# Performance work log

Measured on AMD Instinct MI355X. Metric: run time of the kernel, lower is better.

Reference implementation:

```python
import jax, jax.numpy as jnp
import numpy as np

H, W = 256, 336
FLOW_SCALING = float(max(H, W))  # max(config['loader']['resolution'])
REG_WEIGHT = 0.001               # config['loss']['flow_regul_weight']
B, N = 8, 262144


def setup_inputs() -> dict:
    key = jax.random.key(0)
    k1, k2, k3, k4, k5 = jax.random.split(key, 5)
    # small flow so a reasonable fraction of warped events stays in-bounds
    flow = 0.05 * jax.random.normal(k1, (B, 2, H, W), dtype=jnp.float32)
    ys = jax.random.randint(k2, (B, N), 0, H).astype(jnp.float32)
    xs = jax.random.randint(k3, (B, N), 0, W).astype(jnp.float32)
    ts = jax.random.uniform(k4, (B, N), dtype=jnp.float32)  # normalized timestamps in [0,1]
    pol = jax.random.randint(k5, (B, N), 0, 2)
    # event layout per the code: (ts, y, x, p)
    event_list = jnp.stack([ts, ys, xs, pol.astype(jnp.float32) * 2.0 - 1.0], axis=-1)
    pol_mask = jnp.stack([(pol == 1), (pol == 0)], axis=-1).astype(jnp.float32)  # [B,N,2]
    return {"flow": flow, "event_list": event_list, "pol_mask": pol_mask}


def _get_interpolation(events, event_flow, tref):
    # warped event coords (y, x): [B, N, 2]
    warped = events[:, :, 1:3] + (tref - events[:, :, 0:1]) * event_flow * FLOW_SCALING
    top_y = jnp.floor(warped[:, :, 0:1])
    bot_y = jnp.floor(warped[:, :, 0:1] + 1.0)
    left_x = jnp.floor(warped[:, :, 1:2])
    right_x = jnp.floor(warped[:, :, 1:2] + 1.0)
    # four bilinear corners stacked along event dim -> [B, 4N, 2]
    idx = jnp.concatenate([
        jnp.concatenate([top_y, left_x], -1),
        jnp.concatenate([top_y, right_x], -1),
        jnp.concatenate([bot_y, left_x], -1),
        jnp.concatenate([bot_y, right_x], -1)], axis=1)
    warped4 = jnp.tile(warped, (1, 4, 1))
    weights = jnp.maximum(0.0, 1.0 - jnp.abs(warped4 - idx))
    mask = ((idx[:, :, 0:1] >= 0) & (idx[:, :, 0:1] < H)
            & (idx[:, :, 1:2] >= 0) & (idx[:, :, 1:2] < W)).astype(weights.dtype)
    idx = idx * mask          # unfeasible indices -> 0
    weights = weights * mask  # unfeasible weights -> 0
    flat_idx = (idx[:, :, 0] * W + idx[:, :, 1]).astype(jnp.int32)  # [B, 4N]
    w = jnp.prod(weights, axis=-1, keepdims=True)                    # [B, 4N, 1]
    return flat_idx, w


def _interpolate(flat_idx, weights, polarity_mask):
    # scatter-add bilinear weights into an H*W image, per batch element
    w = (weights * polarity_mask)[:, :, 0]  # [B, 4N]
    return jax.vmap(lambda i, v: jax.ops.segment_sum(v, i, num_segments=H * W))(flat_idx, w)


def reference(flow, event_list, pol_mask):
    pol4 = jnp.tile(pol_mask, (1, 4, 1))              # [B, 4N, 2]
    ts4 = jnp.tile(event_list[:, :, 0:1], (1, 4, 1))  # [B, 4N, 1]
    # gather flow at original event pixel locations
    flow_idx = (event_list[:, :, 1] * W + event_list[:, :, 2]).astype(jnp.int32)  # [B, N]
    flow_flat = flow.reshape(flow.shape[0], 2, -1)
    event_flowy = jnp.take_along_axis(flow_flat[:, 1, :], flow_idx, axis=1)
    event_flowx = jnp.take_along_axis(flow_flat[:, 0, :], flow_idx, axis=1)
    event_flow = jnp.stack([event_flowy, event_flowx], axis=-1)  # [B, N, 2] (y, x)

    loss = jnp.float32(0.0)
    # forward warp (tref=1, avg ts) and backward warp (tref=0, avg 1-ts)
    for tref, tgrad in ((1.0, ts4), (0.0, 1.0 - ts4)):
        idx, wts = _get_interpolation(event_list, event_flow, tref)
        for p in range(2):  # positive / negative polarity
            pm = pol4[:, :, p:p + 1]
            iwe = _interpolate(idx, wts, pm)
            iwe_ts = _interpolate(idx, wts * tgrad, pm)
            loss = loss + jnp.sum((iwe_ts / (iwe + 1e-9)) ** 2)

    # charbonnier flow smoothness
    flow_dx = flow[:, :, :-1, :] - flow[:, :, 1:, :]
    flow_dy = flow[:, :, :, :-1] - flow[:, :, :, 1:]
    smooth = jnp.sum(jnp.sqrt(flow_dx ** 2 + 1e-6)) + jnp.sum(jnp.sqrt(flow_dy ** 2 + 1e-6))
    return loss + REG_WEIGHT * smooth
```

## Files before the change

kernel.cpp:

```cpp
#include <hip/hip_runtime.h>

#define HH 256
#define WW 336
#define HWPIX (HH * WW)
#define BATCH 8
#define NEV 262144
#define NEV_SHIFT 18
#define FLOW_SCALING 336.0f
#define REG_WEIGHT 0.001f

#define BANDS 32
#define BANDSHIFT 3
#define BANDROWS 8
#define NBINS (2 * BATCH * BANDS)
#define CAP 14336
#define GSTRIDE 16

#define BE_THREADS 512
#define EVPT 2
#define EV_PER_BLOCK (BE_THREADS * EVPT)
#define MAXITEMS 4096

#define HTILE (BANDROWS * WW)
#define NBLK_ACC NBINS

#define GCOUNT_BYTES (NBINS * GSTRIDE * 4)
#define ITEMS_BYTES ((size_t)NBINS * CAP * 8)

__device__ __forceinline__ float wave_reduce_sum(float v) {
    #pragma unroll
    for (int o = 32; o > 0; o >>= 1) v += __shfl_down(v, o, 64);
    return v;
}

__device__ __forceinline__ float charb(float d) { return sqrtf(d * d + 1e-6f); }

__global__ __launch_bounds__(256)
void flow_prep(const float* __restrict__ flow,
               unsigned int* __restrict__ gcount, float* __restrict__ loss_acc,
               unsigned int* __restrict__ done_count,
               float* __restrict__ smooth_partial) {
    __shared__ float red[4];
    int tid = threadIdx.x;
    if (blockIdx.x == 0) {
        for (int i = tid; i < NBINS * GSTRIDE; i += 256) gcount[i] = 0u;
        if (tid == 0) { *loss_acc = 0.0f; *done_count = 0u; }
    }

    const int N4 = BATCH * HWPIX / 4;
    const int H4 = HWPIX / 4;
    const int W4 = WW / 4;
    float v = 0.0f;
    for (int i = blockIdx.x * 256 + tid; i < N4; i += gridDim.x * 256) {
        int b = i / H4, u = i - b * H4;
        int row = u / W4, c4 = u - row * W4;
        const float4* ch0 = (const float4*)(flow + (size_t)b * 2 * HWPIX);
        const float4* ch1 = ch0 + H4;
        float4 a0 = ch0[u];
        float4 a1 = ch1[u];

        if (row < HH - 1) {
            float4 d0 = ch0[u + W4];
            float4 d1 = ch1[u + W4];
            v += charb(a0.x - d0.x) + charb(a0.y - d0.y) +
                 charb(a0.z - d0.z) + charb(a0.w - d0.w) +
                 charb(a1.x - d1.x) + charb(a1.y - d1.y) +
                 charb(a1.z - d1.z) + charb(a1.w - d1.w);
        }
        v += charb(a0.x - a0.y) + charb(a0.y - a0.z) + charb(a0.z - a0.w) +
             charb(a1.x - a1.y) + charb(a1.y - a1.z) + charb(a1.z - a1.w);
        if (c4 < W4 - 1) {
            float r0 = ((const float*)ch0)[4 * u + 4];
            float r1 = ((const float*)ch1)[4 * u + 4];
            v += charb(a0.w - r0) + charb(a1.w - r1);
        }
    }
    v = wave_reduce_sum(v);
    if ((tid & 63) == 0) red[tid >> 6] = v;
    __syncthreads();
    if (tid < 4) {
        float r = red[tid];
        r += __shfl_down(r, 2, 64);
        r += __shfl_down(r, 1, 64);
        if (tid == 0) smooth_partial[blockIdx.x] = r;
    }
}

__global__ __launch_bounds__(BE_THREADS)
void bin_events(const float* __restrict__ flow,
                const float4* __restrict__ ev,
                unsigned int* __restrict__ gcount,
                uint2* __restrict__ items) {
    __shared__ int lcnt[64];
    __shared__ int loff[64];
    __shared__ int gbase[64];
    __shared__ int stotal;
    __shared__ __align__(16) unsigned long long sval[MAXITEMS];

    int tid = threadIdx.x;
    if (tid < 64) lcnt[tid] = 0;
    __syncthreads();

    int base = blockIdx.x * EV_PER_BLOCK;
    int b = base >> NEV_SHIFT;
    const float* fxp = flow + (size_t)b * 2 * HWPIX;
    const float* fyp = fxp + HWPIX;

    unsigned int pkv[EVPT][2];
    unsigned int hiA[EVPT][2], hiB[EVPT][2];
    int rkA[EVPT][2], rkB[EVPT][2];

    #pragma unroll
    for (int e = 0; e < EVPT; ++e) {
        int bn = base + e * BE_THREADS + tid;
        float4 ee = ev[bn];
        float t = ee.x, y = ee.y, x = ee.z;
        unsigned int p = (ee.w > 0.0f) ? 0u : 1u;

        int iy = (int)y, ix = (int)x;
        int off = iy * WW + ix;
        float fx = fxp[off];
        float fy = fyp[off];

        #pragma unroll
        for (int tr = 0; tr < 2; ++tr) {
            rkA[e][tr] = -1; rkB[e][tr] = -1;
            float tref  = tr ? 0.0f : 1.0f;
            float tg    = tr ? (1.0f - t) : t;
            float dtS = (tref - t) * FLOW_SCALING;
            float wy = fmaf(dtS, fy, y);
            float wx = fmaf(dtS, fx, x);
            if (!(wx > -1.0f && wx < (float)WW)) continue;
            if (!(wy > -1.0f && wy < (float)HH)) continue;

            int ty = (int)floorf(wy);
            int band0 = -1, band1 = -1;
            if (ty >= 0 && ty < HH) band0 = ty >> BANDSHIFT;
            int r1 = ty + 1;
            if (r1 >= 0 && r1 < HH) {
                int bb = r1 >> BANDSHIFT;
                if (bb != band0) band1 = bb;
            }

            unsigned int qx = (unsigned int)(fmaf(wx, 2048.0f, 2048.5f));
            unsigned int qt = (unsigned int)(tg * 2047.0f + 0.5f);
            pkv[e][tr] = (qx << 12) | (qt << 1) | p;

            if (band0 >= 0) {
                float wyrel = wy - (float)(band0 * BANDROWS - 1);
                unsigned int qy = (unsigned int)fmaf(wyrel, 2048.0f, 0.5f);
                int lb = tr * BANDS + band0;
                hiA[e][tr] = qy | ((unsigned int)lb << 16);
                rkA[e][tr] = atomicAdd(&lcnt[lb], 1);
            }
            if (band1 >= 0) {
                float wyrel = wy - (float)(band1 * BANDROWS - 1);
                unsigned int qy = (unsigned int)fmaf(wyrel, 2048.0f, 0.5f);
                int lb = tr * BANDS + band1;
                hiB[e][tr] = qy | ((unsigned int)lb << 16);
                rkB[e][tr] = atomicAdd(&lcnt[lb], 1);
            }
        }
    }
    __syncthreads();

    if (tid < 64) {
        int c = lcnt[tid];
        int xg = c;
        #pragma unroll
        for (int o = 1; o < 64; o <<= 1) {
            int yv = __shfl_up(xg, o, 64);
            if (tid >= o) xg += yv;
        }
        loff[tid] = xg - c;
        if (tid == 63) stotal = xg;
        int gbin = ((tid >> 5) * BATCH + b) * BANDS + (tid & 31);
        gbase[tid] = c > 0 ? (int)atomicAdd(&gcount[gbin * GSTRIDE],
                                            (unsigned int)c) : 0;
    }
    __syncthreads();

    #pragma unroll
    for (int e = 0; e < EVPT; ++e) {
        #pragma unroll
        for (int tr = 0; tr < 2; ++tr) {
            if (rkA[e][tr] >= 0) {
                int lb = (hiA[e][tr] >> 16) & 63;
                sval[loff[lb] + rkA[e][tr]] =
                    (unsigned long long)pkv[e][tr] |
                    ((unsigned long long)hiA[e][tr] << 32);
            }
            if (rkB[e][tr] >= 0) {
                int lb = (hiB[e][tr] >> 16) & 63;
                sval[loff[lb] + rkB[e][tr]] =
                    (unsigned long long)pkv[e][tr] |
                    ((unsigned long long)hiB[e][tr] << 32);
            }
        }
    }
    __syncthreads();

    int total = stotal;
    for (int i = tid * 2; i < total; i += 2 * BE_THREADS) {
        uint4 two = *(const uint4*)&sval[i];
        unsigned int pk0 = two.x, h0 = two.y;
        unsigned int qy0 = h0 & 0xffffu;
        int lb0 = (h0 >> 16) & 63;
        int gs0 = gbase[lb0] + (i - loff[lb0]);
        int gbin0 = ((lb0 >> 5) * BATCH + b) * BANDS + (lb0 & 31);

        if ((i + 1) < total) {
            unsigned int pk1 = two.z, h1 = two.w;
            unsigned int qy1 = h1 & 0xffffu;
            int lb1 = (h1 >> 16) & 63;
            int gs1 = gbase[lb1] + (i + 1 - loff[lb1]);
            if (lb1 == lb0 && (gs0 & 1) == 0 && gs1 < CAP) {
                *(uint4*)(items + (size_t)gbin0 * CAP + gs0) =
                    make_uint4(pk0, qy0, pk1, qy1);
                continue;
            }
            int gbin1 = ((lb1 >> 5) * BATCH + b) * BANDS + (lb1 & 31);
            if (gs1 < CAP) items[(size_t)gbin1 * CAP + gs1] = make_uint2(pk1, qy1);
        }
        if (gs0 < CAP) items[(size_t)gbin0 * CAP + gs0] = make_uint2(pk0, qy0);
    }
}

__device__ __forceinline__ unsigned int pack_w(float w, float tg) {
    unsigned int lo16 = (unsigned int)fmaf(w, 1024.0f, 0.5f);
    unsigned int hi16 = (unsigned int)fmaf(w * tg, 1024.0f, 0.5f);
    return lo16 | (hi16 << 16);
}

__device__ __forceinline__ void accum_item(unsigned int* __restrict__ sA,
                                           unsigned int* __restrict__ sB,
                                           unsigned int pk, unsigned int qy) {
    float wx = (float)(pk >> 12) * (1.0f / 2048.0f) - 1.0f;
    float tg = (float)((pk >> 1) & 2047u) * (1.0f / 2047.0f);
    int p = pk & 1u;

    int rowq = qy >> 11;
    float fy = (float)(qy & 2047u) * (1.0f / 2048.0f);
    int row_top = rowq - 1;

    float lxf = floorf(wx);
    float fxx = wx - lxf;
    int lx = (int)lxf;

    unsigned int* A  = sA + p * HTILE;
    unsigned int* Bb = sB + p * HTILE;

    #pragma unroll
    for (int a = 0; a < 2; ++a) {
        int ry = row_top + a;
        if ((unsigned)ry >= (unsigned)BANDROWS) continue;
        float wrow = a ? fy : (1.0f - fy);
        int rb = ry * WW;
        if (lx >= 0 && lx + 1 < WW) {
            unsigned int pl = pack_w(wrow * (1.0f - fxx), tg);
            unsigned int pr = pack_w(wrow * fxx, tg);
            unsigned long long v =
                (unsigned long long)pl | ((unsigned long long)pr << 32);
            if ((lx & 1) == 0) {
                atomicAdd((unsigned long long*)(A + rb + lx), v);
            } else {
                atomicAdd((unsigned long long*)(Bb + rb + lx - 1), v);
            }
        } else if (lx == -1) {
            atomicAdd(&A[rb], pack_w(wrow * fxx, tg));
        } else if (lx == WW - 1) {
            atomicAdd(&A[rb + lx], pack_w(wrow * (1.0f - fxx), tg));
        }
    }
}

__global__ __launch_bounds__(1024)
void bin_accum(const unsigned int* __restrict__ gcount,
               const uint2* __restrict__ items,
               const float* __restrict__ smooth_partial,
               float* __restrict__ loss_acc,
               unsigned int* __restrict__ done_count,
               float* __restrict__ out) {
    __shared__ __align__(16) unsigned int sA[2 * HTILE];
    __shared__ __align__(16) unsigned int sB[2 * HTILE];
    __shared__ float red[16];
    __shared__ int lastflag;

    int band = blockIdx.x;
    int tr   = blockIdx.y;
    int b    = blockIdx.z;
    int tid  = threadIdx.x;

    for (int i = tid; i < 2 * HTILE; i += 1024) { sA[i] = 0u; sB[i] = 0u; }
    __syncthreads();

    int gbin = (tr * BATCH + b) * BANDS + band;
    int cnt = min((int)gcount[gbin * GSTRIDE], CAP);
    const uint2* bp = items + (size_t)gbin * CAP;
    const uint4* bp4 = (const uint4*)bp;

    int nquad = cnt >> 2;
    for (int n = tid; n < nquad; n += 1024) {
        uint4 c0 = bp4[2 * n];
        uint4 c1 = bp4[2 * n + 1];
        accum_item(sA, sB, c0.x, c0.y);
        accum_item(sA, sB, c0.z, c0.w);
        accum_item(sA, sB, c1.x, c1.y);
        accum_item(sA, sB, c1.z, c1.w);
    }
    int rem = cnt & 3;
    if (tid < rem) {
        uint2 u = bp[nquad * 4 + tid];
        accum_item(sA, sB, u.x, u.y);
    }
    __syncthreads();

    float v = 0.0f;
    for (int i = tid; i < 2 * HTILE; i += 1024) {
        int px = i - (i / WW) * WW;
        unsigned int u = sA[i] + (px ? sB[i - 1] : 0u);
        float iwe = (float)(u & 0xffffu);
        float its = (float)(u >> 16);
        float r = its / (iwe + 1.024e-6f);
        v += r * r;
    }
    v = wave_reduce_sum(v);
    if ((tid & 63) == 0) red[tid >> 6] = v;
    __syncthreads();
    if (tid == 0) {
        float r = 0.0f;
        #pragma unroll
        for (int k = 0; k < 16; ++k) r += red[k];
        atomicAdd(loss_acc, r);
        __threadfence();
        unsigned int t = atomicAdd(done_count, 1u);
        lastflag = (t == (unsigned)(NBLK_ACC - 1));
    }
    __syncthreads();

    if (lastflag) {
        float pv = (tid < 512) ? smooth_partial[tid] : 0.0f;
        pv = wave_reduce_sum(pv);
        if ((tid & 63) == 0) red[tid >> 6] = pv;
        __syncthreads();
        if (tid == 0) {
            float sm = 0.0f;
            #pragma unroll
            for (int k = 0; k < 16; ++k) sm += red[k];
            float total = atomicAdd(loss_acc, 0.0f);
            *out = total + REG_WEIGHT * sm;
        }
    }
}

extern "C" void kernel_launch(void* const* d_in, const int* in_sizes, int n_in,
                              void* d_out, int out_size, void* d_ws, size_t ws_size,
                              hipStream_t stream) {
    const float*  flow  = (const float*)d_in[0];
    const float4* ev    = (const float4*)d_in[1];
    float* out = (float*)d_out;

    unsigned int* gcount     = (unsigned int*)d_ws;
    float*        loss_acc   = (float*)((char*)d_ws + GCOUNT_BYTES);
    unsigned int* done_count = (unsigned int*)((char*)d_ws + GCOUNT_BYTES + 4);
    float*        smooth_p   = (float*)((char*)d_ws + GCOUNT_BYTES + 512);
    uint2*        items      = (uint2*)((char*)d_ws + GCOUNT_BYTES + 4096);

    flow_prep<<<512, 256, 0, stream>>>(flow, gcount, loss_acc,
                                       done_count, smooth_p);

    int total_ev = BATCH * NEV;
    bin_events<<<total_ev / EV_PER_BLOCK, BE_THREADS, 0, stream>>>(
        flow, ev, gcount, items);

    dim3 g2(BANDS, 2, BATCH);
    bin_accum<<<g2, 1024, 0, stream>>>(gcount, items, smooth_p, loss_acc,
                                       done_count, out);
}
```

Baseline: 149.1 us.

## Fold smoothness into accumulate kernel, memset workspace, larger binning blocks, padded bins

```diff
diff --git a/kernel.cpp b/kernel.cpp
--- a/kernel.cpp
+++ b/kernel.cpp
@@ -16,15 +16,16 @@
 #define CAP 14336
 #define GSTRIDE 16
 
-#define BE_THREADS 512
+#define BE_THREADS 1024
 #define EVPT 2
 #define EV_PER_BLOCK (BE_THREADS * EVPT)
-#define MAXITEMS 4096
+#define MAXITEMS 8320
 
 #define HTILE (BANDROWS * WW)
 #define NBLK_ACC NBINS
 
 #define GCOUNT_BYTES (NBINS * GSTRIDE * 4)
+#define ZERO_BYTES 33024
 #define ITEMS_BYTES ((size_t)NBINS * CAP * 8)
 
 __device__ __forceinline__ float wave_reduce_sum(float v) {
@@ -34,57 +35,6 @@
 }
 
 __device__ __forceinline__ float charb(float d) { return sqrtf(d * d + 1e-6f); }
-
-__global__ __launch_bounds__(256)
-void flow_prep(const float* __restrict__ flow,
-               unsigned int* __restrict__ gcount, float* __restrict__ loss_acc,
-               unsigned int* __restrict__ done_count,
-               float* __restrict__ smooth_partial) {
-    __shared__ float red[4];
-    int tid = threadIdx.x;
-    if (blockIdx.x == 0) {
-        for (int i = tid; i < NBINS * GSTRIDE; i += 256) gcount[i] = 0u;
-        if (tid == 0) { *loss_acc = 0.0f; *done_count = 0u; }
-    }
-
-    const int N4 = BATCH * HWPIX / 4;
-    const int H4 = HWPIX / 4;
-    const int W4 = WW / 4;
-    float v = 0.0f;
-    for (int i = blockIdx.x * 256 + tid; i < N4; i += gridDim.x * 256) {
-        int b = i / H4, u = i - b * H4;
-        int row = u / W4, c4 = u - row * W4;
-        const float4* ch0 = (const float4*)(flow + (size_t)b * 2 * HWPIX);
-        const float4* ch1 = ch0 + H4;
-        float4 a0 = ch0[u];
-        float4 a1 = ch1[u];
-
-        if (row < HH - 1) {
-            float4 d0 = ch0[u + W4];
-            float4 d1 = ch1[u + W4];
-            v += charb(a0.x - d0.x) + charb(a0.y - d0.y) +
-                 charb(a0.z - d0.z) + charb(a0.w - d0.w) +
-                 charb(a1.x - d1.x) + charb(a1.y - d1.y) +
-                 charb(a1.z - d1.z) + charb(a1.w - d1.w);
-        }
-        v += charb(a0.x - a0.y) + charb(a0.y - a0.z) + charb(a0.z - a0.w) +
-             charb(a1.x - a1.y) + charb(a1.y - a1.z) + charb(a1.z - a1.w);
-        if (c4 < W4 - 1) {
-            float r0 = ((const float*)ch0)[4 * u + 4];
-            float r1 = ((const float*)ch1)[4 * u + 4];
-            v += charb(a0.w - r0) + charb(a1.w - r1);
-        }
-    }
-    v = wave_reduce_sum(v);
-    if ((tid & 63) == 0) red[tid >> 6] = v;
-    __syncthreads();
-    if (tid < 4) {
-        float r = red[tid];
-        r += __shfl_down(r, 2, 64);
-        r += __shfl_down(r, 1, 64);
-        if (tid == 0) smooth_partial[blockIdx.x] = r;
-    }
-}
 
 __global__ __launch_bounds__(BE_THREADS)
 void bin_events(const float* __restrict__ flow,
@@ -165,18 +115,24 @@
     __syncthreads();
 
     if (tid < 64) {
-        int c = lcnt[tid];
-        int xg = c;
+        int c  = lcnt[tid];
+        int ce = (c + 1) & ~1;
+        int xg = ce;
         #pragma unroll
         for (int o = 1; o < 64; o <<= 1) {
             int yv = __shfl_up(xg, o, 64);
             if (tid >= o) xg += yv;
         }
-        loff[tid] = xg - c;
+        int lo = xg - ce;
+        loff[tid] = lo;
         if (tid == 63) stotal = xg;
         int gbin = ((tid >> 5) * BATCH + b) * BANDS + (tid & 31);
-        gbase[tid] = c > 0 ? (int)atomicAdd(&gcount[gbin * GSTRIDE],
-                                            (unsigned int)c) : 0;
+        gbase[tid] = ce > 0 ? (int)atomicAdd(&gcount[gbin * GSTRIDE],
+                                             (unsigned int)ce) : 0;
+        if (c & 1) {
+            unsigned int hi = (15u << 11) | ((unsigned int)tid << 16);
+            sval[lo + c] = ((unsigned long long)hi << 32);
+        }
     }
     __syncthreads();
 
@@ -275,9 +231,9 @@
 }
 
 __global__ __launch_bounds__(1024)
-void bin_accum(const unsigned int* __restrict__ gcount,
+void bin_accum(const float* __restrict__ flow,
+               const unsigned int* __restrict__ gcount,
                const uint2* __restrict__ items,
-               const float* __restrict__ smooth_partial,
                float* __restrict__ loss_acc,
                unsigned int* __restrict__ done_count,
                float* __restrict__ out) {
@@ -290,6 +246,7 @@
     int tr   = blockIdx.y;
     int b    = blockIdx.z;
     int tid  = threadIdx.x;
+    int lblk = band + 32 * (tr + 2 * b);
 
     for (int i = tid; i < 2 * HTILE; i += 1024) { sA[i] = 0u; sB[i] = 0u; }
     __syncthreads();
@@ -300,9 +257,18 @@
     const uint4* bp4 = (const uint4*)bp;
 
     int nquad = cnt >> 2;
-    for (int n = tid; n < nquad; n += 1024) {
-        uint4 c0 = bp4[2 * n];
-        uint4 c1 = bp4[2 * n + 1];
+    if (tid < nquad) {
+        uint4 c0 = bp4[2 * tid];
+        uint4 c1 = bp4[2 * tid + 1];
+        for (int n = tid + 1024; n < nquad; n += 1024) {
+            uint4 d0 = bp4[2 * n];
+            uint4 d1 = bp4[2 * n + 1];
+            accum_item(sA, sB, c0.x, c0.y);
+            accum_item(sA, sB, c0.z, c0.w);
+            accum_item(sA, sB, c1.x, c1.y);
+            accum_item(sA, sB, c1.z, c1.w);
+            c0 = d0; c1 = d1;
+        }
         accum_item(sA, sB, c0.x, c0.y);
         accum_item(sA, sB, c0.z, c0.w);
         accum_item(sA, sB, c1.x, c1.y);
@@ -312,6 +278,36 @@
     if (tid < rem) {
         uint2 u = bp[nquad * 4 + tid];
         accum_item(sA, sB, u.x, u.y);
+    }
+
+    float sm = 0.0f;
+    {
+        const int N4 = BATCH * HWPIX / 4;
+        const int H4 = HWPIX / 4;
+        const int W4 = WW / 4;
+        for (int i = lblk * 1024 + tid; i < N4; i += NBLK_ACC * 1024) {
+            int bb = i / H4, u = i - bb * H4;
+            int row = u / W4, c4 = u - row * W4;
+            const float4* ch0 = (const float4*)(flow + (size_t)bb * 2 * HWPIX);
+            const float4* ch1 = ch0 + H4;
+            float4 a0 = ch0[u];
+            float4 a1 = ch1[u];
+            if (row < HH - 1) {
+                float4 d0 = ch0[u + W4];
+                float4 d1 = ch1[u + W4];
+                sm += charb(a0.x - d0.x) + charb(a0.y - d0.y) +
+                      charb(a0.z - d0.z) + charb(a0.w - d0.w) +
+                      charb(a1.x - d1.x) + charb(a1.y - d1.y) +
+                      charb(a1.z - d1.z) + charb(a1.w - d1.w);
+            }
+            sm += charb(a0.x - a0.y) + charb(a0.y - a0.z) + charb(a0.z - a0.w) +
+                  charb(a1.x - a1.y) + charb(a1.y - a1.z) + charb(a1.z - a1.w);
+            if (c4 < W4 - 1) {
+                float r0 = ((const float*)ch0)[4 * u + 4];
+                float r1 = ((const float*)ch1)[4 * u + 4];
+                sm += charb(a0.w - r0) + charb(a1.w - r1);
+            }
+        }
     }
     __syncthreads();
 
@@ -324,6 +320,7 @@
         float r = its / (iwe + 1.024e-6f);
         v += r * r;
     }
+    v = fmaf(sm, REG_WEIGHT, v);
     v = wave_reduce_sum(v);
     if ((tid & 63) == 0) red[tid >> 6] = v;
     __syncthreads();
@@ -338,18 +335,8 @@
     }
     __syncthreads();
 
-    if (lastflag) {
-        float pv = (tid < 512) ? smooth_partial[tid] : 0.0f;
-        pv = wave_reduce_sum(pv);
-        if ((tid & 63) == 0) red[tid >> 6] = pv;
-        __syncthreads();
-        if (tid == 0) {
-            float sm = 0.0f;
-            #pragma unroll
-            for (int k = 0; k < 16; ++k) sm += red[k];
-            float total = atomicAdd(loss_acc, 0.0f);
-            *out = total + REG_WEIGHT * sm;
-        }
+    if (lastflag && tid == 0) {
+        *out = atomicAdd(loss_acc, 0.0f);
     }
 }
 
@@ -363,17 +350,15 @@
     unsigned int* gcount     = (unsigned int*)d_ws;
     float*        loss_acc   = (float*)((char*)d_ws + GCOUNT_BYTES);
     unsigned int* done_count = (unsigned int*)((char*)d_ws + GCOUNT_BYTES + 4);
-    float*        smooth_p   = (float*)((char*)d_ws + GCOUNT_BYTES + 512);
     uint2*        items      = (uint2*)((char*)d_ws + GCOUNT_BYTES + 4096);
 
-    flow_prep<<<512, 256, 0, stream>>>(flow, gcount, loss_acc,
-                                       done_count, smooth_p);
+    hipMemsetAsync(d_ws, 0, ZERO_BYTES, stream);
 
     int total_ev = BATCH * NEV;
     bin_events<<<total_ev / EV_PER_BLOCK, BE_THREADS, 0, stream>>>(
         flow, ev, gcount, items);
 
     dim3 g2(BANDS, 2, BATCH);
-    bin_accum<<<g2, 1024, 0, stream>>>(gcount, items, smooth_p, loss_acc,
+    bin_accum<<<g2, 1024, 0, stream>>>(flow, gcount, items, loss_acc,
                                        done_count, out);
 }
```

Measured after the change: 138.3 us. 1.08x faster.
